# Optimization experiments

Measured on AMD Instinct MI355X. Metric: run time of the kernel, lower is better.

Reference implementation:

```python
import jax, jax.numpy as jnp
import numpy as np
from jax.ops import segment_sum, segment_max

DIM = 64
NUM_FEAT = 14
EDGE_FEAT = 4
OUT_DIM = 16
NUM_GRAPHS = 512
NEG_SLOPE = 0.01


def _leaky(v):
    return jnp.where(v >= 0, v, NEG_SLOPE * v)


def setup_inputs() -> dict:
    key = jax.random.key(0)
    ks = jax.random.split(key, 24)
    N, E = 20000, 40000
    s = 0.1
    inp = {
        "x": jax.random.normal(ks[0], (N, NUM_FEAT), jnp.float32),
        "edge_attr": jax.random.normal(ks[1], (E, EDGE_FEAT), jnp.float32),
        "edge_index": jax.random.randint(ks[2], (2, E), 0, N, jnp.int64) if jax.config.jax_enable_x64 else jax.random.randint(ks[2], (2, E), 0, N).astype(jnp.int32),
        "batch": jnp.sort(jax.random.randint(ks[3], (N,), 0, NUM_GRAPHS)).astype(jnp.int32),
        # lin0
        "lin0_w": s * jax.random.normal(ks[4], (DIM, NUM_FEAT), jnp.float32),
        "lin0_b": s * jax.random.normal(ks[5], (DIM,), jnp.float32),
        # edge network: Linear(4,dim) -> LeakyReLU -> Linear(dim, dim*dim)
        "net_w1": s * jax.random.normal(ks[6], (DIM, EDGE_FEAT), jnp.float32),
        "net_b1": s * jax.random.normal(ks[7], (DIM,), jnp.float32),
        "net_w2": s * jax.random.normal(ks[8], (DIM * DIM, DIM), jnp.float32),
        "net_b2": s * jax.random.normal(ks[9], (DIM * DIM,), jnp.float32),
        # NNConv root weight + bias
        "root_w": s * jax.random.normal(ks[10], (DIM, DIM), jnp.float32),
        "conv_b": s * jax.random.normal(ks[11], (DIM,), jnp.float32),
        # GRU (torch gate order: r, z, n)
        "gru_w_ih": s * jax.random.normal(ks[12], (3 * DIM, DIM), jnp.float32),
        "gru_w_hh": s * jax.random.normal(ks[13], (3 * DIM, DIM), jnp.float32),
        "gru_b_ih": s * jax.random.normal(ks[14], (3 * DIM,), jnp.float32),
        "gru_b_hh": s * jax.random.normal(ks[15], (3 * DIM,), jnp.float32),
        # Set2Set LSTM (input 2*dim, hidden dim; torch gate order: i, f, g, o)
        "lstm_w_ih": s * jax.random.normal(ks[16], (4 * DIM, 2 * DIM), jnp.float32),
        "lstm_w_hh": s * jax.random.normal(ks[17], (4 * DIM, DIM), jnp.float32),
        "lstm_b_ih": s * jax.random.normal(ks[18], (4 * DIM,), jnp.float32),
        "lstm_b_hh": s * jax.random.normal(ks[19], (4 * DIM,), jnp.float32),
        # lin_out
        "lout_w": s * jax.random.normal(ks[20], (OUT_DIM, 2 * DIM), jnp.float32),
        "lout_b": s * jax.random.normal(ks[21], (OUT_DIM,), jnp.float32),
    }
    return inp


def _forward(x, edge_attr, lin0_w, lin0_b, net_w1, net_b1, net_w2, net_b2,
             root_w, conv_b, gru_w_ih, gru_w_hh, gru_b_ih, gru_b_hh,
             lstm_w_ih, lstm_w_hh, lstm_b_ih, lstm_b_hh, lout_w, lout_b,
             edge_index, batch):
    N = x.shape[0]
    src, tgt = edge_index[0], edge_index[1]

    # per-edge dim x dim weight (shared across the 6 steps; edge_attr is static)
    ew = _leaky(edge_attr @ net_w1.T + net_b1) @ net_w2.T + net_b2  # [E, dim*dim]
    ew = ew.reshape(-1, DIM, DIM)  # [E, in, out]

    deg = segment_sum(jnp.ones_like(tgt, jnp.float32), tgt, num_segments=N)
    inv_deg = 1.0 / jnp.maximum(deg, 1.0)

    out = _leaky(x @ lin0_w.T + lin0_b)  # [N, dim]
    h = out
    for _ in range(6):
        msg = jnp.einsum('ed,edo->eo', out[src], ew)  # gather + per-edge matvec
        agg = segment_sum(msg, tgt, num_segments=N) * inv_deg[:, None]  # scatter-mean
        conv = agg + out @ root_w + conv_b
        m = _leaky(conv)
        # GRU cell (seq len 1)
        gi = m @ gru_w_ih.T + gru_b_ih
        gh = h @ gru_w_hh.T + gru_b_hh
        gi_r, gi_z, gi_n = jnp.split(gi, 3, axis=-1)
        gh_r, gh_z, gh_n = jnp.split(gh, 3, axis=-1)
        r = jax.nn.sigmoid(gi_r + gh_r)
        z = jax.nn.sigmoid(gi_z + gh_z)
        n = jnp.tanh(gi_n + r * gh_n)
        h = (1.0 - z) * n + z * h
        out = h

    # Set2Set, processing_steps=1
    B = NUM_GRAPHS
    q_star = jnp.zeros((B, 2 * DIM), x.dtype)
    h_l = jnp.zeros((B, DIM), x.dtype)
    c_l = jnp.zeros((B, DIM), x.dtype)
    gates = q_star @ lstm_w_ih.T + lstm_b_ih + h_l @ lstm_w_hh.T + lstm_b_hh
    gi_, gf_, gg_, go_ = jnp.split(gates, 4, axis=-1)
    i_g = jax.nn.sigmoid(gi_)
    f_g = jax.nn.sigmoid(gf_)
    g_g = jnp.tanh(gg_)
    o_g = jax.nn.sigmoid(go_)
    c = f_g * c_l + i_g * g_g
    q = o_g * jnp.tanh(c)  # [B, dim]

    e = jnp.sum(out * q[batch], axis=-1)  # [N]
    emax = segment_max(e, batch, num_segments=B)
    emax = jnp.where(jnp.isfinite(emax), emax, 0.0)
    ex = jnp.exp(e - emax[batch])
    denom = segment_sum(ex, batch, num_segments=B)
    a = ex / jnp.maximum(denom, 1e-16)[batch]
    r_read = segment_sum(a[:, None] * out, batch, num_segments=B)  # [B, dim]
    q_star = jnp.concatenate([q, r_read], axis=-1)  # [B, 2*dim]

    return q_star @ lout_w.T + lout_b  # [B, out_dim]


def reference(x, edge_attr, edge_index, batch, lin0_w, lin0_b, net_w1, net_b1,
              net_w2, net_b2, root_w, conv_b, gru_w_ih, gru_w_hh, gru_b_ih,
              gru_b_hh, lstm_w_ih, lstm_w_hh, lstm_b_ih, lstm_b_hh, lout_w, lout_b):
    return _forward(x, edge_attr, lin0_w, lin0_b, net_w1, net_b1, net_w2, net_b2,
                    root_w, conv_b, gru_w_ih, gru_w_hh, gru_b_ih, gru_b_hh,
                    lstm_w_ih, lstm_w_hh, lstm_b_ih, lstm_b_hh, lout_w, lout_b,
                    edge_index, batch)
```

## Files before the change

kernel.cpp:

```cpp
#include <hip/hip_runtime.h>
#include <math.h>

#define DIM 64
#define NFEAT 14
#define EFEAT 4
#define ODIM 16
#define NGRAPH 512
#define NEG 0.01f
#define EBLK 128
#define DSPLIT 4

typedef _Float16 f16;
typedef _Float16 f16x8 __attribute__((ext_vector_type(8)));
typedef float f32x4 __attribute__((ext_vector_type(4)));

#define MFMA(a,b,c) __builtin_amdgcn_mfma_f32_16x16x32_f16(a,b,c,0,0,0)

__device__ __forceinline__ float leaky(float v){ return v >= 0.f ? v : NEG*v; }
__device__ __forceinline__ float sigm(float v){ return 1.f/(1.f+expf(-v)); }

__global__ void k_pack(const float* __restrict__ src, f16* __restrict__ dst, int NC, int transB){
    int i = blockIdx.x*blockDim.x + threadIdx.x;
    if (i >= NC*64) return;
    int j = i & 7, l = (i >> 3) & 63, s = (i >> 9) & 1, CT = i >> 10;
    int k = ((l >> 4) << 3) + 32*s + j;
    int c = CT*16 + (l & 15);
    float v = transB ? src[(size_t)k*NC + c] : src[(size_t)c*64 + k];
    dst[i] = (f16)v;
}

__global__ void k_hid(const float* __restrict__ ea, const float* __restrict__ w1,
                      const float* __restrict__ b1, f16* __restrict__ hid16, int E){
    int i = blockIdx.x*blockDim.x + threadIdx.x;
    if (i >= E*DIM) return;
    int e = i >> 6, k = i & 63;
    const float* a = ea + (size_t)e*EFEAT;
    const float* w = w1 + k*EFEAT;
    float v = b1[k] + a[0]*w[0] + a[1]*w[1] + a[2]*w[2] + a[3]*w[3];
    hid16[i] = (f16)leaky(v);
}

__global__ void k_deg(const int* __restrict__ ei, float* __restrict__ deg, int E){
    int e = blockIdx.x*blockDim.x + threadIdx.x;
    if (e < E) atomicAdd(&deg[ei[E + e]], 1.0f);
}

__global__ void k_invdeg(float* __restrict__ deg, int N){
    int i = blockIdx.x*blockDim.x + threadIdx.x;
    if (i < N) deg[i] = 1.0f / fmaxf(deg[i], 1.0f);
}

__global__ void k_lin0(const float* __restrict__ x, const float* __restrict__ w,
                       const float* __restrict__ b, float* __restrict__ hf,
                       f16* __restrict__ out16, int N){
    int i = blockIdx.x*blockDim.x + threadIdx.x;
    if (i >= N*DIM) return;
    int n = i >> 6, o = i & 63;
    const float* xr = x + (size_t)n*NFEAT;
    const float* wr = w + o*NFEAT;
    float v = b[o];
#pragma unroll
    for (int f = 0; f < NFEAT; ++f) v += xr[f]*wr[f];
    v = leaky(v);
    hf[i] = v; out16[i] = (f16)v;
}

__global__ __launch_bounds__(256) void k_nbias(const f16x8* __restrict__ out16v,
                                               const f16x8* __restrict__ b2f,
                                               float* __restrict__ nb, int N){
    int n0 = blockIdx.x*64;
    int tid = threadIdx.x, w = tid >> 6, l = tid & 63, li = l & 15, lh = l >> 4;
    int ar = n0 + 16*w + li;
    f16x8 a0{}, a1{};
    if (ar < N){ a0 = out16v[(size_t)ar*8 + lh]; a1 = out16v[(size_t)ar*8 + lh + 4]; }
    f32x4 z = {0.f,0.f,0.f,0.f};
#pragma unroll
    for (int ct = 0; ct < 4; ++ct){
        f32x4 p = MFMA(a0, b2f[(ct*2+0)*64 + l], z);
        p = MFMA(a1, b2f[(ct*2+1)*64 + l], p);
#pragma unroll
        for (int reg = 0; reg < 4; ++reg){
            int n = n0 + 16*w + lh*4 + reg;
            if (n < N) nb[(size_t)n*64 + ct*16 + li] = p[reg];
        }
    }
}

__global__ __launch_bounds__(256) void k_fmsg(const float* __restrict__ hf,
                                              const f16x8* __restrict__ hid16v,
                                              const f16x8* __restrict__ wpf,
                                              const float* __restrict__ nb,
                                              const int* __restrict__ ei,
                                              float* __restrict__ agg, int E){
    __shared__ f16x8 Wlds[2048];
    __shared__ f16 OsT[EBLK][24];
    __shared__ int ssrc[EBLK];
    __shared__ int stgt[EBLK];
    int tid = threadIdx.x;
    int e0 = blockIdx.x*EBLK;
    int dbase = blockIdx.y*16;
    if (tid < EBLK){
        int e = e0 + tid;
        ssrc[tid] = (e < E) ? ei[e] : -1;
        stgt[tid] = (e < E) ? ei[E + e] : -1;
    }
    __syncthreads();
    {
        int r = tid >> 1, half = tid & 1;
        int s = ssrc[r];
        float tmpf[8] = {0.f,0.f,0.f,0.f,0.f,0.f,0.f,0.f};
        if (s >= 0){
            const float4* hp = (const float4*)(hf + (size_t)s*64 + dbase + half*8);
            *(float4*)&tmpf[0] = hp[0];
            *(float4*)&tmpf[4] = hp[1];
        }
        f16 tmph[8];
#pragma unroll
        for (int j = 0; j < 8; ++j) tmph[j] = (f16)tmpf[j];
        *(f16x8*)&OsT[r][half*8] = *(f16x8*)&tmph[0];
    }

    int w = tid >> 6, l = tid & 63, li = l & 15, lh = l >> 4;
    f16x8 a[2][2];
#pragma unroll
    for (int rt = 0; rt < 2; ++rt){
        int e = e0 + w*32 + rt*16 + li;
        if (e < E){
            a[rt][0] = hid16v[(size_t)e*8 + lh];
            a[rt][1] = hid16v[(size_t)e*8 + lh + 4];
        } else { a[rt][0] = f16x8{}; a[rt][1] = f16x8{}; }
    }

    f16x8 p[8];
    {
        const f16x8* src = wpf + (size_t)dbase*512;
#pragma unroll
        for (int i = 0; i < 8; ++i) p[i] = src[tid + i*256];
    }

    f32x4 acc[2][4] = {};

    for (int c = 0; c < 4; ++c){
        __syncthreads();
#pragma unroll
        for (int i = 0; i < 8; ++i) Wlds[tid + i*256] = p[i];
        __syncthreads();
        if (c < 3){
            const f16x8* src = wpf + (size_t)(dbase + (c+1)*4)*512;
#pragma unroll
            for (int i = 0; i < 8; ++i) p[i] = src[tid + i*256];
        }
#pragma unroll
        for (int dd = 0; dd < 4; ++dd){
            int dl = c*4 + dd;
            f16 s0 = OsT[w*32 + li][dl];
            f16 s1 = OsT[w*32 + 16 + li][dl];
            f16x8 as00 = a[0][0]*s0, as01 = a[0][1]*s0;
            f16x8 as10 = a[1][0]*s1, as11 = a[1][1]*s1;
#pragma unroll
            for (int ct = 0; ct < 4; ++ct){
                f16x8 b0 = Wlds[(dd*8 + ct*2 + 0)*64 + l];
                f16x8 b1 = Wlds[(dd*8 + ct*2 + 1)*64 + l];
                acc[0][ct] = MFMA(as00, b0, acc[0][ct]);
                acc[0][ct] = MFMA(as01, b1, acc[0][ct]);
                acc[1][ct] = MFMA(as10, b0, acc[1][ct]);
                acc[1][ct] = MFMA(as11, b1, acc[1][ct]);
            }
        }
    }

#pragma unroll
    for (int rt = 0; rt < 2; ++rt){
#pragma unroll
        for (int reg = 0; reg < 4; ++reg){
            int row = w*32 + rt*16 + lh*4 + reg;
            int t = stgt[row];
            if (t < 0) continue;
            int s = ssrc[row];
#pragma unroll
            for (int ct = 0; ct < 4; ++ct){
                int col = ct*16 + li;
                float v = acc[rt][ct][reg];
                if (blockIdx.y == 0) v += nb[(size_t)s*64 + col];
                atomicAdd(&agg[(size_t)t*64 + col], v);
            }
        }
    }
}

__global__ __launch_bounds__(256) void k_node(float* __restrict__ hf,
                                              f16* __restrict__ out16,
                                              const f16x8* __restrict__ out16v,
                                              float* __restrict__ agg,
                                              const float* __restrict__ invdeg,
                                              const float* __restrict__ convb,
                                              const f16x8* __restrict__ wrf,
                                              const f16x8* __restrict__ wihf,
                                              const f16x8* __restrict__ whhf,
                                              const float* __restrict__ bih,
                                              const float* __restrict__ bhh,
                                              const f16x8* __restrict__ b2f,
                                              float* __restrict__ nb, int N){
    __shared__ f16 Ms[64][72];
    int n0 = blockIdx.x*64;
    int tid = threadIdx.x, w = tid >> 6, l = tid & 63, li = l & 15, lh = l >> 4;
    f32x4 z = {0.f,0.f,0.f,0.f};

    int ar = n0 + 16*w + li;
    f16x8 a0{}, a1{};
    if (ar < N){ a0 = out16v[(size_t)ar*8 + lh]; a1 = out16v[(size_t)ar*8 + lh + 4]; }

    int nrow[4]; float invd[4];
#pragma unroll
    for (int reg = 0; reg < 4; ++reg){
        nrow[reg] = n0 + 16*w + lh*4 + reg;
        invd[reg] = (nrow[reg] < N) ? invdeg[nrow[reg]] : 0.f;
    }

#pragma unroll
    for (int ct = 0; ct < 4; ++ct){
        f32x4 p = MFMA(a0, wrf[(ct*2+0)*64 + l], z);
        p = MFMA(a1, wrf[(ct*2+1)*64 + l], p);
        int col = ct*16 + li;
        float cb = convb[col];
#pragma unroll
        for (int reg = 0; reg < 4; ++reg){
            int n = nrow[reg];
            float m = 0.f;
            if (n < N){
                size_t idx = (size_t)n*64 + col;
                m = leaky(p[reg] + agg[idx]*invd[reg] + cb);
                agg[idx] = 0.f;
            }
            Ms[16*w + lh*4 + reg][col] = (f16)m;
        }
    }

    f16x8 am0 = *(const f16x8*)&Ms[16*w + li][lh*8];
    f16x8 am1 = *(const f16x8*)&Ms[16*w + li][lh*8 + 32];

#pragma unroll
    for (int ctq = 0; ctq < 4; ++ctq){
        int col = ctq*16 + li;
        f32x4 pir = MFMA(am0, wihf[((ctq+0)*2+0)*64 + l], z);
        pir = MFMA(am1, wihf[((ctq+0)*2+1)*64 + l], pir);
        f32x4 piz = MFMA(am0, wihf[((ctq+4)*2+0)*64 + l], z);
        piz = MFMA(am1, wihf[((ctq+4)*2+1)*64 + l], piz);
        f32x4 pin = MFMA(am0, wihf[((ctq+8)*2+0)*64 + l], z);
        pin = MFMA(am1, wihf[((ctq+8)*2+1)*64 + l], pin);
        f32x4 phr = MFMA(a0, whhf[((ctq+0)*2+0)*64 + l], z);
        phr = MFMA(a1, whhf[((ctq+0)*2+1)*64 + l], phr);
        f32x4 phz = MFMA(a0, whhf[((ctq+4)*2+0)*64 + l], z);
        phz = MFMA(a1, whhf[((ctq+4)*2+1)*64 + l], phz);
        f32x4 phn = MFMA(a0, whhf[((ctq+8)*2+0)*64 + l], z);
        phn = MFMA(a1, whhf[((ctq+8)*2+1)*64 + l], phn);
        float bir = bih[col], biz = bih[64+col], bin = bih[128+col];
        float bhr = bhh[col], bhz = bhh[64+col], bhn = bhh[128+col];
#pragma unroll
        for (int reg = 0; reg < 4; ++reg){
            int n = nrow[reg];
            float hnew = 0.f;
            if (n < N){
                float hv = hf[(size_t)n*64 + col];
                float r  = sigm(pir[reg] + bir + phr[reg] + bhr);
                float zz = sigm(piz[reg] + biz + phz[reg] + bhz);
                float nn = tanhf(pin[reg] + bin + r*(phn[reg] + bhn));
                hnew = (1.f - zz)*nn + zz*hv;
                hf[(size_t)n*64 + col] = hnew;
                out16[(size_t)n*64 + col] = (f16)hnew;
            }
            Ms[16*w + lh*4 + reg][col] = (f16)hnew;
        }
    }

    f16x8 an0 = *(const f16x8*)&Ms[16*w + li][lh*8];
    f16x8 an1 = *(const f16x8*)&Ms[16*w + li][lh*8 + 32];
#pragma unroll
    for (int ct = 0; ct < 4; ++ct){
        f32x4 p = MFMA(an0, b2f[(ct*2+0)*64 + l], z);
        p = MFMA(an1, b2f[(ct*2+1)*64 + l], p);
#pragma unroll
        for (int reg = 0; reg < 4; ++reg){
            int n = nrow[reg];
            if (n < N) nb[(size_t)n*64 + ct*16 + li] = p[reg];
        }
    }
}

__global__ void k_q(const float* __restrict__ bih, const float* __restrict__ bhh,
                    float* __restrict__ q){
    int j = threadIdx.x;
    if (j >= 64) return;
    float gi = bih[j]       + bhh[j];
    float gg = bih[128+j]   + bhh[128+j];
    float go = bih[192+j]   + bhh[192+j];
    float c = sigm(gi)*tanhf(gg);
    q[j] = sigm(go)*tanhf(c);
}

__device__ __forceinline__ unsigned fkey(float f){
    unsigned u = __float_as_uint(f);
    return (u >> 31) ? ~u : (u | 0x80000000u);
}

__global__ void k_edot(const float* __restrict__ out, const float* __restrict__ q,
                       const int* __restrict__ batch, float* __restrict__ ebuf,
                       unsigned* __restrict__ emaxk, int N){
    int gw = (blockIdx.x*blockDim.x + threadIdx.x) >> 6;
    int d = threadIdx.x & 63;
    if (gw >= N) return;
    float v = out[(size_t)gw*64 + d] * q[d];
#pragma unroll
    for (int s = 32; s; s >>= 1) v += __shfl_xor(v, s, 64);
    if (d == 0){
        ebuf[gw] = v;
        atomicMax(&emaxk[batch[gw]], fkey(v));
    }
}

__global__ void k_ex(float* __restrict__ ebuf, const unsigned* __restrict__ emaxk,
                     const int* __restrict__ batch, float* __restrict__ denom, int N){
    int n = blockIdx.x*blockDim.x + threadIdx.x;
    if (n >= N) return;
    int b = batch[n];
    unsigned k = emaxk[b];
    float em = (k == 0u) ? 0.f
             : ((k >> 31) ? __uint_as_float(k ^ 0x80000000u) : __uint_as_float(~k));
    float ex = expf(ebuf[n] - em);
    ebuf[n] = ex;
    atomicAdd(&denom[b], ex);
}

__global__ void k_rr(const float* __restrict__ out, const float* __restrict__ ebuf,
                     const float* __restrict__ denom, const int* __restrict__ batch,
                     float* __restrict__ rr, int N){
    int gw = (blockIdx.x*blockDim.x + threadIdx.x) >> 6;
    int o = threadIdx.x & 63;
    if (gw >= N) return;
    int b = batch[gw];
    float a = ebuf[gw] / fmaxf(denom[b], 1e-16f);
    atomicAdd(&rr[(size_t)b*64 + o], a * out[(size_t)gw*64 + o]);
}

__global__ void k_out(const float* __restrict__ q, const float* __restrict__ rr,
                      const float* __restrict__ lw, const float* __restrict__ lb,
                      float* __restrict__ dout){
    int i = blockIdx.x*blockDim.x + threadIdx.x;
    if (i >= NGRAPH*ODIM) return;
    int b = i / ODIM, j = i % ODIM;
    const float* w = lw + j*128;
    float acc = lb[j];
#pragma unroll 8
    for (int d = 0; d < 64; ++d) acc += w[d]*q[d];
    const float* rb = rr + (size_t)b*64;
#pragma unroll 8
    for (int d = 0; d < 64; ++d) acc += w[64+d]*rb[d];
    dout[i] = acc;
}

extern "C" void kernel_launch(void* const* d_in, const int* in_sizes, int n_in,
                              void* d_out, int out_size, void* d_ws, size_t ws_size,
                              hipStream_t stream){
    const float* x     = (const float*)d_in[0];
    const float* ea    = (const float*)d_in[1];
    const int*   ei    = (const int*)  d_in[2];
    const int*   batch = (const int*)  d_in[3];
    const float* lin0w = (const float*)d_in[4];
    const float* lin0b = (const float*)d_in[5];
    const float* w1    = (const float*)d_in[6];
    const float* b1    = (const float*)d_in[7];
    const float* w2    = (const float*)d_in[8];
    const float* b2    = (const float*)d_in[9];
    const float* rootw = (const float*)d_in[10];
    const float* convb = (const float*)d_in[11];
    const float* gwih  = (const float*)d_in[12];
    const float* gwhh  = (const float*)d_in[13];
    const float* gbih  = (const float*)d_in[14];
    const float* gbhh  = (const float*)d_in[15];
    const float* lsbih = (const float*)d_in[18];
    const float* lsbhh = (const float*)d_in[19];
    const float* loutw = (const float*)d_in[20];
    const float* loutb = (const float*)d_in[21];

    int N = in_sizes[0] / NFEAT;
    int E = in_sizes[1] / EFEAT;

    char* p = (char*)d_ws;
    size_t off = 0;
    auto carve = [&](size_t bytes) -> void* {
        void* r = p + off;
        off += (bytes + 255) & ~(size_t)255;
        return r;
    };
    f16*      hid16  = (f16*)     carve((size_t)E*64*2);
    float*    hf     = (float*)   carve((size_t)N*64*4);
    f16*      out16  = (f16*)     carve((size_t)N*64*2);
    float*    nb     = (float*)   carve((size_t)N*64*4);
    float*    qv     = (float*)   carve(64*4);
    float*    ebuf   = (float*)   carve((size_t)N*4);
    f16*      wpf    = (f16*)     carve((size_t)4096*64*2);
    f16*      wrf    = (f16*)     carve(64*64*2);
    f16*      b2f    = (f16*)     carve(64*64*2);
    f16*      wihf   = (f16*)     carve(192*64*2);
    f16*      whhf   = (f16*)     carve(192*64*2);
    size_t zero_beg = off;
    float*    agg    = (float*)   carve((size_t)N*64*4);
    float*    invdeg = (float*)   carve((size_t)N*4);
    unsigned* emaxk  = (unsigned*)carve(NGRAPH*4);
    float*    denom  = (float*)   carve(NGRAPH*4);
    float*    rr     = (float*)   carve((size_t)NGRAPH*64*4);
    size_t zero_end = off;

    hipMemsetAsync(p + zero_beg, 0, zero_end - zero_beg, stream);

    k_pack<<<(4096*64 + 255)/256, 256, 0, stream>>>(w2,    wpf,  4096, 0);
    k_pack<<<(64*64   + 255)/256, 256, 0, stream>>>(rootw, wrf,  64,   1);
    k_pack<<<(64*64   + 255)/256, 256, 0, stream>>>(b2,    b2f,  64,   1);
    k_pack<<<(192*64  + 255)/256, 256, 0, stream>>>(gwih,  wihf, 192,  0);
    k_pack<<<(192*64  + 255)/256, 256, 0, stream>>>(gwhh,  whhf, 192,  0);

    k_hid<<<((size_t)E*64 + 255)/256, 256, 0, stream>>>(ea, w1, b1, hid16, E);
    k_deg<<<(E + 255)/256, 256, 0, stream>>>(ei, invdeg, E);
    k_invdeg<<<(N + 255)/256, 256, 0, stream>>>(invdeg, N);
    k_lin0<<<((size_t)N*64 + 255)/256, 256, 0, stream>>>(x, lin0w, lin0b, hf, out16, N);

    int eb  = (E + EBLK - 1)/EBLK;
    int nbk = (N + 63)/64;
    int node_grid = ((size_t)N*64 + 255)/256;

    k_nbias<<<nbk, 256, 0, stream>>>((const f16x8*)out16, (const f16x8*)b2f, nb, N);
    for (int it = 0; it < 6; ++it){
        k_fmsg<<<dim3(eb, DSPLIT), 256, 0, stream>>>(hf, (const f16x8*)hid16,
                                                     (const f16x8*)wpf, nb, ei, agg, E);
        k_node<<<nbk, 256, 0, stream>>>(hf, out16, (const f16x8*)out16, agg, invdeg,
                                        convb, (const f16x8*)wrf, (const f16x8*)wihf,
                                        (const f16x8*)whhf, gbih, gbhh,
                                        (const f16x8*)b2f, nb, N);
    }

    k_q<<<1, 64, 0, stream>>>(lsbih, lsbhh, qv);
    k_edot<<<node_grid, 256, 0, stream>>>(hf, qv, batch, ebuf, emaxk, N);
    k_ex<<<(N + 255)/256, 256, 0, stream>>>(ebuf, emaxk, batch, denom, N);
    k_rr<<<node_grid, 256, 0, stream>>>(hf, ebuf, denom, batch, rr, N);
    k_out<<<(NGRAPH*ODIM + 255)/256, 256, 0, stream>>>(qv, rr, loutw, loutb, (float*)d_out);
}
```

Before: 536.9 us.

## Repartition edge-message MFMA work so each wave owns one output column tile

Each wave in the edge kernel now covers all 128 edges of the block for one 16-column output tile, where before it covered 32 edges across all 64 columns. Each wave therefore reads only two weight fragments from LDS per d step instead of eight. Source-feature scalars are fetched as vectors into registers every other chunk rather than one scalar LDS load per step. In exchange each thread holds 16 activation fragments and does more f16 scaling multiplies, which raises register pressure and may lower occupancy.

Result: slower. 608.2 us (+13.3%).

```diff
diff --git a/kernel.cpp b/kernel.cpp
--- a/kernel.cpp
+++ b/kernel.cpp
@@ -106,25 +106,25 @@
     }
     __syncthreads();
     {
-        int r = tid >> 1, half = tid & 1;
+        int r = tid >> 1, dh = tid & 1;
         int s = ssrc[r];
         float tmpf[8] = {0.f,0.f,0.f,0.f,0.f,0.f,0.f,0.f};
         if (s >= 0){
-            const float4* hp = (const float4*)(hf + (size_t)s*64 + dbase + half*8);
+            const float4* hp = (const float4*)(hf + (size_t)s*64 + dbase + dh*8);
             *(float4*)&tmpf[0] = hp[0];
             *(float4*)&tmpf[4] = hp[1];
         }
         f16 tmph[8];
 #pragma unroll
         for (int j = 0; j < 8; ++j) tmph[j] = (f16)tmpf[j];
-        *(f16x8*)&OsT[r][half*8] = *(f16x8*)&tmph[0];
+        *(f16x8*)&OsT[r][dh*8] = *(f16x8*)&tmph[0];
     }
 
     int w = tid >> 6, l = tid & 63, li = l & 15, lh = l >> 4;
-    f16x8 a[2][2];
-#pragma unroll
-    for (int rt = 0; rt < 2; ++rt){
-        int e = e0 + w*32 + rt*16 + li;
+    f16x8 a[8][2];
+#pragma unroll
+    for (int rt = 0; rt < 8; ++rt){
+        int e = e0 + rt*16 + li;
         if (e < E){
             a[rt][0] = hid16v[(size_t)e*8 + lh];
             a[rt][1] = hid16v[(size_t)e*8 + lh + 4];
@@ -138,8 +138,10 @@
         for (int i = 0; i < 8; ++i) p[i] = src[tid + i*256];
     }
 
-    f32x4 acc[2][4] = {};
-
+    f32x4 acc[8] = {};
+    f16x8 osr[8];
+
+#pragma unroll
     for (int c = 0; c < 4; ++c){
         __syncthreads();
 #pragma unroll
@@ -150,40 +152,37 @@
 #pragma unroll
             for (int i = 0; i < 8; ++i) p[i] = src[tid + i*256];
         }
+        if ((c & 1) == 0){
+#pragma unroll
+            for (int rt = 0; rt < 8; ++rt)
+                osr[rt] = *(const f16x8*)&OsT[rt*16 + li][(c >> 1)*8];
+        }
 #pragma unroll
         for (int dd = 0; dd < 4; ++dd){
-            int dl = c*4 + dd;
-            f16 s0 = OsT[w*32 + li][dl];
-            f16 s1 = OsT[w*32 + 16 + li][dl];
-            f16x8 as00 = a[0][0]*s0, as01 = a[0][1]*s0;
-            f16x8 as10 = a[1][0]*s1, as11 = a[1][1]*s1;
-#pragma unroll
-            for (int ct = 0; ct < 4; ++ct){
-                f16x8 b0 = Wlds[(dd*8 + ct*2 + 0)*64 + l];
-                f16x8 b1 = Wlds[(dd*8 + ct*2 + 1)*64 + l];
-                acc[0][ct] = MFMA(as00, b0, acc[0][ct]);
-                acc[0][ct] = MFMA(as01, b1, acc[0][ct]);
-                acc[1][ct] = MFMA(as10, b0, acc[1][ct]);
-                acc[1][ct] = MFMA(as11, b1, acc[1][ct]);
+            const int dl = c*4 + dd;
+            f16x8 b0 = Wlds[(dd*8 + w*2 + 0)*64 + l];
+            f16x8 b1 = Wlds[(dd*8 + w*2 + 1)*64 + l];
+#pragma unroll
+            for (int rt = 0; rt < 8; ++rt){
+                f16 s = osr[rt][dl & 7];
+                acc[rt] = MFMA(a[rt][0]*s, b0, acc[rt]);
+                acc[rt] = MFMA(a[rt][1]*s, b1, acc[rt]);
             }
         }
     }
 
 #pragma unroll
-    for (int rt = 0; rt < 2; ++rt){
+    for (int rt = 0; rt < 8; ++rt){
 #pragma unroll
         for (int reg = 0; reg < 4; ++reg){
-            int row = w*32 + rt*16 + lh*4 + reg;
+            int row = rt*16 + lh*4 + reg;
             int t = stgt[row];
             if (t < 0) continue;
             int s = ssrc[row];
-#pragma unroll
-            for (int ct = 0; ct < 4; ++ct){
-                int col = ct*16 + li;
-                float v = acc[rt][ct][reg];
-                if (blockIdx.y == 0) v += nb[(size_t)s*64 + col];
-                atomicAdd(&agg[(size_t)t*64 + col], v);
-            }
+            int col = w*16 + li;
+            float v = acc[rt][reg];
+            if (blockIdx.y == 0) v += nb[(size_t)s*64 + col];
+            atomicAdd(&agg[(size_t)t*64 + col], v);
         }
     }
 }
```
